# Performance work log

Hardware: AMD Instinct MI355X
Metric: run time of the kernel (lower is better)

Reference implementation:

```python
import jax, jax.numpy as jnp
import numpy as np

ALPHA = 0.2  # LeakyReLU negative slope


def setup_inputs() -> dict:
    key = jax.random.key(0)
    k1, k2, k3, k4 = jax.random.split(key, 4)
    B, W, N = 128, 128, 512  # batch, window_size, n_features
    x = jax.random.normal(k1, (B, W, N), dtype=jnp.float32)
    W_fc = jax.random.normal(k2, (W, W), dtype=jnp.float32) * (1.0 / np.sqrt(W))
    b_fc = jax.random.normal(k3, (W,), dtype=jnp.float32) * 0.01
    attn = jax.random.normal(k4, (2 * W, 1), dtype=jnp.float32) * (1.414 / np.sqrt(2 * W))
    return {"x": x, "W_fc": W_fc, "b_fc": b_fc, "attn": attn}


def reference(x, W_fc, b_fc, attn):
    # x: (B, window_size, n_features)
    Wsz = attn.shape[0] // 2
    xp = jnp.transpose(x, (0, 2, 1))                 # (B, N, W)
    h = jnp.einsum('bnw,vw->bnv', xp, W_fc) + b_fc   # fc over window dim: (B, N, W)
    # Split-projection equivalent of concat([x_i, h_j]) @ attn:
    a1 = attn[:Wsz, 0]
    a2 = attn[Wsz:, 0]
    s1 = xp @ a1                                     # (B, N) -- x_i part (repeat_interleave)
    s2 = h @ a2                                      # (B, N) -- h_j part (repeat)
    e = jax.nn.leaky_relu(s1[:, :, None] + s2[:, None, :], negative_slope=ALPHA)  # (B, N, N)
    attention = jax.nn.softmax(e, axis=2)            # softmax over j
    # dropout is identity in eval mode (train=False)
    out = jax.nn.sigmoid(jnp.einsum('bij,bjw->biw', attention, xp))  # (B, N, W)
    return jnp.transpose(out, (0, 2, 1))             # (B, W, N)
```

## Files before the change

kernel.cpp:

```cpp
#include <hip/hip_runtime.h>

#define Bb 128
#define Ww 128
#define Nn 512
#define ALPHA 0.2f
#define LOG2E 1.44269504088896340736f

typedef __attribute__((ext_vector_type(8))) short short8;
typedef __attribute__((ext_vector_type(4))) float f32x4;

__device__ __forceinline__ unsigned pk_bf16(float lo, float hi) {
  unsigned r;
  asm("v_cvt_pk_bf16_f32 %0, %1, %2" : "=v"(r) : "v"(lo), "v"(hi));
  return r;
}

__device__ __forceinline__ float v_exp2(float x) {
  float r;
  asm("v_exp_f32 %0, %1" : "=v"(r) : "v"(x));
  return r;
}

__device__ __forceinline__ float v_rcp(float x) {
  float r;
  asm("v_rcp_f32 %0, %1" : "=v"(r) : "v"(x));
  return r;
}

#define T_OFF   0
#define T_BYTES (64 * 129 * 8 * 2)
#define SR_OFF  (T_OFF + T_BYTES)
#define S1_OFF  (SR_OFF + 16384)
#define S2_OFF  (S1_OFF + 2048)
#define CV_OFF  (S2_OFF + 2048)
#define SMEM12  (CV_OFF + 528)

__launch_bounds__(1024, 1)
__global__ void attn_k(const float* __restrict__ x, const float* __restrict__ Wfc,
                       const float* __restrict__ bfc, const float* __restrict__ attn,
                       float* __restrict__ out) {
  extern __shared__ char smem[];
  ushort* tile = (ushort*)(smem + T_OFF);
  float*  sred = (float*)(smem + SR_OFF);
  float*  s1s  = (float*)(smem + S1_OFF);
  float*  s2s  = (float*)(smem + S2_OFF);
  float*  cvs  = (float*)(smem + CV_OFF);

  const int bid = blockIdx.x;
  const int xcd = bid & 7, idx = bid >> 3;
  const int b  = xcd * 16 + (idx >> 1);
  const int i0 = (idx & 1) * 256;
  const int t  = threadIdx.x;
  const int wvw = t >> 6;
  const int lane = t & 63;
  const int wl = lane & 15, lg = lane >> 4;
  const int g  = t >> 7;
  const int q2 = t & 127;
  const float* xb = x + (size_t)b * (Ww * Nn);

  {
    const int wcol = t & 127, vq = t >> 7;
    float p = 0.f;
#pragma unroll
    for (int vi = 0; vi < 16; ++vi) {
      const int v = vq * 16 + vi;
      p = fmaf(attn[Ww + v], Wfc[v * Ww + wcol], p);
    }
    sred[t] = p;
    if (t < 64) {
      float c0p = fmaf(bfc[t], attn[Ww + t], bfc[t + 64] * attn[Ww + 64 + t]);
#pragma unroll
      for (int off = 32; off; off >>= 1) c0p += __shfl_xor(c0p, off);
      if (t == 0) cvs[Ww] = c0p;
    }
  }
  __syncthreads();
  if (t < Ww) {
    float s = 0.f;
#pragma unroll
    for (int j = 0; j < 8; ++j) s += sred[t + 128 * j];
    cvs[t] = s;
  }
  __syncthreads();

  float s1p[4] = {0.f, 0.f, 0.f, 0.f};
  float s2p[4] = {0.f, 0.f, 0.f, 0.f};
  {
    float4 L[16];
#pragma unroll
    for (int k = 0; k < 16; ++k)
      L[k] = *reinterpret_cast<const float4*>(xb + (size_t)(g + 8 * k) * Nn + 4 * q2);
#pragma unroll
    for (int k = 0; k < 16; ++k) {
      const int w = g + 8 * k;
      const float aw = attn[w];
      const float cw = cvs[w];
      const float4 v = L[k];
      s1p[0] = fmaf(v.x, aw, s1p[0]); s1p[1] = fmaf(v.y, aw, s1p[1]);
      s1p[2] = fmaf(v.z, aw, s1p[2]); s1p[3] = fmaf(v.w, aw, s1p[3]);
      s2p[0] = fmaf(v.x, cw, s2p[0]); s2p[1] = fmaf(v.y, cw, s2p[1]);
      s2p[2] = fmaf(v.z, cw, s2p[2]); s2p[3] = fmaf(v.w, cw, s2p[3]);
      uint2 pk;
      pk.x = pk_bf16(v.x, v.y);
      pk.y = pk_bf16(v.z, v.w);
      *reinterpret_cast<uint2*>(tile + ((size_t)(q2 >> 1) * 129 + w) * 8 + (q2 & 1) * 4) = pk;
    }
  }

  *reinterpret_cast<f32x4*>(&sred[t * 4]) = (f32x4){s1p[0], s1p[1], s1p[2], s1p[3]};
  __syncthreads();
  float red = 0.f;
  if (t < 512) {
#pragma unroll
    for (int j = 0; j < 8; ++j) red += sred[j * 512 + t];
  }
  __syncthreads();
  if (t < 512) s1s[t] = red * LOG2E;
  *reinterpret_cast<f32x4*>(&sred[t * 4]) = (f32x4){s2p[0], s2p[1], s2p[2], s2p[3]};
  __syncthreads();
  if (t < 512) {
    float d = 0.f;
#pragma unroll
    for (int j = 0; j < 8; ++j) d += sred[j * 512 + t];
    s2s[t] = (d + cvs[Ww]) * LOG2E;
  }
  __syncthreads();

  const float s1i = s1s[i0 + wvw * 16 + wl];

  f32x4 acc[8];
  f32x4 accl = (f32x4){0.f, 0.f, 0.f, 0.f};
#pragma unroll
  for (int f = 0; f < 8; ++f) acc[f] = (f32x4){0.f, 0.f, 0.f, 0.f};
  short8 ones;
#pragma unroll
  for (int e = 0; e < 8; ++e) ones[e] = (short)0x3F80;

  for (int jj = 0; jj < 16; ++jj) {
    const int jb = jj * 32 + 8 * lg;
    float sv[8];
    *reinterpret_cast<float4*>(&sv[0]) = *reinterpret_cast<const float4*>(&s2s[jb]);
    *reinterpret_cast<float4*>(&sv[4]) = *reinterpret_cast<const float4*>(&s2s[jb + 4]);
    float p[8];
#pragma unroll
    for (int e = 0; e < 8; ++e) {
      const float u = s1i + sv[e];
      p[e] = v_exp2(fmaxf(u, ALPHA * u));
    }
    short8 af;
    unsigned* au = reinterpret_cast<unsigned*>(&af);
    au[0] = pk_bf16(p[0], p[1]); au[1] = pk_bf16(p[2], p[3]);
    au[2] = pk_bf16(p[4], p[5]); au[3] = pk_bf16(p[6], p[7]);

    const ushort* tb = tile + (size_t)(jj * 4 + lg) * 129 * 8;
#pragma unroll
    for (int f = 0; f < 8; ++f) {
      const short8 bfr = *reinterpret_cast<const short8*>(tb + (16 * f + wl) * 8);
      acc[f] = __builtin_amdgcn_mfma_f32_16x16x32_bf16(af, bfr, acc[f], 0, 0, 0);
    }
    accl = __builtin_amdgcn_mfma_f32_16x16x32_bf16(af, ones, accl, 0, 0, 0);
  }

  float invl[4];
#pragma unroll
  for (int m = 0; m < 4; ++m) invl[m] = LOG2E * v_rcp(accl[m]);
  const int ibase = i0 + wvw * 16 + lg * 4;
  float* outb = out + (size_t)b * (Ww * Nn);
#pragma unroll
  for (int f = 0; f < 8; ++f) {
    float4 o;
    o.x = v_rcp(1.f + v_exp2(-(acc[f][0] * invl[0])));
    o.y = v_rcp(1.f + v_exp2(-(acc[f][1] * invl[1])));
    o.z = v_rcp(1.f + v_exp2(-(acc[f][2] * invl[2])));
    o.w = v_rcp(1.f + v_exp2(-(acc[f][3] * invl[3])));
    *reinterpret_cast<float4*>(outb + (16 * f + wl) * Nn + ibase) = o;
  }
}

extern "C" void kernel_launch(void* const* d_in, const int* in_sizes, int n_in,
                              void* d_out, int out_size, void* d_ws, size_t ws_size,
                              hipStream_t stream) {
  const float* x    = (const float*)d_in[0];
  const float* Wfc  = (const float*)d_in[1];
  const float* bfc  = (const float*)d_in[2];
  const float* attn = (const float*)d_in[3];
  float* out = (float*)d_out;

  (void)hipFuncSetAttribute(reinterpret_cast<const void*>(&attn_k),
                            hipFuncAttributeMaxDynamicSharedMemorySize, SMEM12);
  attn_k<<<256, 1024, SMEM12, stream>>>(x, Wfc, bfc, attn, out);
}
```

Before: 26.38 us.

## Issue x and W_fc loads up front and overlap the c-vector reduction

Issues the W_fc loads and the x tile loads at kernel start, before any barrier, so global memory latency overlaps with computing the attention projection vector. The s1 reduction, bf16 tile packing and c-vector partial sums now share one barrier. s2 is computed afterwards from the x values still held in registers, which removes one __syncthreads. A separate shared buffer for the c-vector partials adds some LDS use and raises register pressure from holding wreg and L together.

New measurement: 25.89 us, median of 3. Within noise of the previous version (-1.9%).

```diff
diff --git a/kernel.cpp b/kernel.cpp
--- a/kernel.cpp
+++ b/kernel.cpp
@@ -33,18 +33,20 @@
 #define S1_OFF  (SR_OFF + 16384)
 #define S2_OFF  (S1_OFF + 2048)
 #define CV_OFF  (S2_OFF + 2048)
-#define SMEM12  (CV_OFF + 528)
+#define CP_OFF  (CV_OFF + 528)
+#define SMEM13  (CP_OFF + 4096)
 
 __launch_bounds__(1024, 1)
-__global__ void attn_k(const float* __restrict__ x, const float* __restrict__ Wfc,
+__global__ void attn_m(const float* __restrict__ x, const float* __restrict__ Wfc,
                        const float* __restrict__ bfc, const float* __restrict__ attn,
                        float* __restrict__ out) {
   extern __shared__ char smem[];
-  ushort* tile = (ushort*)(smem + T_OFF);
-  float*  sred = (float*)(smem + SR_OFF);
-  float*  s1s  = (float*)(smem + S1_OFF);
-  float*  s2s  = (float*)(smem + S2_OFF);
-  float*  cvs  = (float*)(smem + CV_OFF);
+  ushort* tile  = (ushort*)(smem + T_OFF);
+  float*  sred  = (float*)(smem + SR_OFF);
+  float*  s1s   = (float*)(smem + S1_OFF);
+  float*  s2s   = (float*)(smem + S2_OFF);
+  float*  cvs   = (float*)(smem + CV_OFF);
+  float*  cpart = (float*)(smem + CP_OFF);
 
   const int bid = blockIdx.x;
   const int xcd = bid & 7, idx = bid >> 3;
@@ -58,57 +60,57 @@
   const int q2 = t & 127;
   const float* xb = x + (size_t)b * (Ww * Nn);
 
+  float wreg[16];
+#pragma unroll
+  for (int vi = 0; vi < 16; ++vi)
+    wreg[vi] = Wfc[(size_t)(g * 16 + vi) * Ww + q2];
+  float c0p = 0.f;
+  if (t < 64)
+    c0p = fmaf(bfc[t], attn[Ww + t], bfc[t + 64] * attn[Ww + 64 + t]);
+  __builtin_amdgcn_sched_barrier(0);
+
+  float4 L[16];
+#pragma unroll
+  for (int k = 0; k < 16; ++k)
+    L[k] = *reinterpret_cast<const float4*>(xb + (size_t)(g + 8 * k) * Nn + 4 * q2);
+  __builtin_amdgcn_sched_barrier(0);
+
   {
-    const int wcol = t & 127, vq = t >> 7;
-    float p = 0.f;
-#pragma unroll
-    for (int vi = 0; vi < 16; ++vi) {
-      const int v = vq * 16 + vi;
-      p = fmaf(attn[Ww + v], Wfc[v * Ww + wcol], p);
+    float cp = 0.f;
+#pragma unroll
+    for (int vi = 0; vi < 16; ++vi)
+      cp = fmaf(attn[Ww + g * 16 + vi], wreg[vi], cp);
+    cpart[t] = cp;
+    if (t < 64) {
+      float cc = c0p;
+#pragma unroll
+      for (int off = 32; off; off >>= 1) cc += __shfl_xor(cc, off);
+      if (t == 0) cvs[Ww] = cc;
     }
-    sred[t] = p;
-    if (t < 64) {
-      float c0p = fmaf(bfc[t], attn[Ww + t], bfc[t + 64] * attn[Ww + 64 + t]);
-#pragma unroll
-      for (int off = 32; off; off >>= 1) c0p += __shfl_xor(c0p, off);
-      if (t == 0) cvs[Ww] = c0p;
-    }
-  }
-  __syncthreads();
+  }
+
+  float s1p[4] = {0.f, 0.f, 0.f, 0.f};
+#pragma unroll
+  for (int k = 0; k < 16; ++k) {
+    const int w = g + 8 * k;
+    const float aw = attn[w];
+    const float4 v = L[k];
+    s1p[0] = fmaf(v.x, aw, s1p[0]); s1p[1] = fmaf(v.y, aw, s1p[1]);
+    s1p[2] = fmaf(v.z, aw, s1p[2]); s1p[3] = fmaf(v.w, aw, s1p[3]);
+    uint2 pk;
+    pk.x = pk_bf16(v.x, v.y);
+    pk.y = pk_bf16(v.z, v.w);
+    *reinterpret_cast<uint2*>(tile + ((size_t)(q2 >> 1) * 129 + w) * 8 + (q2 & 1) * 4) = pk;
+  }
+  *reinterpret_cast<f32x4*>(&sred[t * 4]) = (f32x4){s1p[0], s1p[1], s1p[2], s1p[3]};
+  __syncthreads();
+
   if (t < Ww) {
     float s = 0.f;
 #pragma unroll
-    for (int j = 0; j < 8; ++j) s += sred[t + 128 * j];
+    for (int j = 0; j < 8; ++j) s += cpart[t + 128 * j];
     cvs[t] = s;
   }
-  __syncthreads();
-
-  float s1p[4] = {0.f, 0.f, 0.f, 0.f};
-  float s2p[4] = {0.f, 0.f, 0.f, 0.f};
-  {
-    float4 L[16];
-#pragma unroll
-    for (int k = 0; k < 16; ++k)
-      L[k] = *reinterpret_cast<const float4*>(xb + (size_t)(g + 8 * k) * Nn + 4 * q2);
-#pragma unroll
-    for (int k = 0; k < 16; ++k) {
-      const int w = g + 8 * k;
-      const float aw = attn[w];
-      const float cw = cvs[w];
-      const float4 v = L[k];
-      s1p[0] = fmaf(v.x, aw, s1p[0]); s1p[1] = fmaf(v.y, aw, s1p[1]);
-      s1p[2] = fmaf(v.z, aw, s1p[2]); s1p[3] = fmaf(v.w, aw, s1p[3]);
-      s2p[0] = fmaf(v.x, cw, s2p[0]); s2p[1] = fmaf(v.y, cw, s2p[1]);
-      s2p[2] = fmaf(v.z, cw, s2p[2]); s2p[3] = fmaf(v.w, cw, s2p[3]);
-      uint2 pk;
-      pk.x = pk_bf16(v.x, v.y);
-      pk.y = pk_bf16(v.z, v.w);
-      *reinterpret_cast<uint2*>(tile + ((size_t)(q2 >> 1) * 129 + w) * 8 + (q2 & 1) * 4) = pk;
-    }
-  }
-
-  *reinterpret_cast<f32x4*>(&sred[t * 4]) = (f32x4){s1p[0], s1p[1], s1p[2], s1p[3]};
-  __syncthreads();
   float red = 0.f;
   if (t < 512) {
 #pragma unroll
@@ -116,6 +118,16 @@
   }
   __syncthreads();
   if (t < 512) s1s[t] = red * LOG2E;
+
+  float s2p[4] = {0.f, 0.f, 0.f, 0.f};
+#pragma unroll
+  for (int k = 0; k < 16; ++k) {
+    const int w = g + 8 * k;
+    const float cw = cvs[w];
+    const float4 v = L[k];
+    s2p[0] = fmaf(v.x, cw, s2p[0]); s2p[1] = fmaf(v.y, cw, s2p[1]);
+    s2p[2] = fmaf(v.z, cw, s2p[2]); s2p[3] = fmaf(v.w, cw, s2p[3]);
+  }
   *reinterpret_cast<f32x4*>(&sred[t * 4]) = (f32x4){s2p[0], s2p[1], s2p[2], s2p[3]};
   __syncthreads();
   if (t < 512) {
@@ -186,7 +198,7 @@
   const float* attn = (const float*)d_in[3];
   float* out = (float*)d_out;
 
-  (void)hipFuncSetAttribute(reinterpret_cast<const void*>(&attn_k),
-                            hipFuncAttributeMaxDynamicSharedMemorySize, SMEM12);
-  attn_k<<<256, 1024, SMEM12, stream>>>(x, Wfc, bfc, attn, out);
-}
+  (void)hipFuncSetAttribute(reinterpret_cast<const void*>(&attn_m),
+                            hipFuncAttributeMaxDynamicSharedMemorySize, SMEM13);
+  attn_m<<<256, 1024, SMEM13, stream>>>(x, Wfc, bfc, attn, out);
+}
```
